# Kernel optimization log

Hardware: AMD Instinct MI355X
Metric: run time of the kernel (lower is better)

## Reference

```python
import jax, jax.numpy as jnp
import numpy as np

# Sizes
N, E = 100000, 3200000
F_NODE, F_EDGE, LD, HID, L = 4, 4, 6, 16, 8
ALPHA = 1.0
EPS = 1e-6


def setup_inputs() -> dict:
    key = jax.random.key(0)
    ks = jax.random.split(key, 8)
    x = jax.random.normal(ks[0], (N, F_NODE), jnp.float32)
    fixed_mask = jax.random.uniform(ks[1], (N,)) < 0.1
    x = x.at[:, -1].set(jnp.where(fixed_mask, jnp.abs(x[:, -1]) + 1.0, 0.0))
    # positive edge attributes (pipe resistance etc.)
    edge_attr = jax.random.uniform(ks[2], (E, F_EDGE), jnp.float32) * 0.9 + 0.1
    edge_index = jax.random.randint(ks[3], (2, E), 0, N, dtype=jnp.int64)
    d_in = 2 * LD + 2 * F_NODE + F_EDGE  # 24: [x_src, x_dst, attr_src, attr_dst, edge_attr]
    s = 0.1
    W1 = jax.random.normal(ks[4], (L, d_in, HID), jnp.float32) * s
    b1 = jnp.zeros((L, HID), jnp.float32)
    W2 = jax.random.normal(ks[5], (L, HID, LD), jnp.float32) * s
    b2 = jnp.zeros((L, LD), jnp.float32)
    Wf = jax.random.normal(ks[6], (LD, 1), jnp.float32) * s
    bf = jnp.zeros((1,), jnp.float32)
    return {"x": x, "edge_attr": edge_attr, "edge_index": edge_index,
            "W1": W1, "b1": b1, "W2": W2, "b2": b2, "Wf": Wf, "bf": bf}


def reference(x, edge_attr, edge_index, W1, b1, W2, b2, Wf, bf):
    src, dst = edge_index[0], edge_index[1]
    # in-degree for mean aggregation
    deg = jax.ops.segment_sum(jnp.ones((E,), jnp.float32), dst, num_segments=N)
    deg = jnp.maximum(deg, 1.0)
    X = jnp.zeros((N, LD), jnp.float32)
    na_src, na_dst = x[src], x[dst]  # static node-attr gathers reused each layer
    for l in range(L):  # num_convs GNNSConv layers
        m_in = jnp.concatenate([X[src], X[dst], na_src, na_dst, edge_attr], axis=-1)  # [E,24]
        h = jax.nn.relu(m_in @ W1[l] + b1[l])         # per-edge MLP hidden [E,16]
        m = h @ W2[l] + b2[l]                          # per-edge message [E,6]
        agg = jax.ops.segment_sum(m, dst, num_segments=N) / deg[:, None]  # mean aggr
        X = (1.0 - ALPHA) * X + ALPHA * agg            # latent update (alpha_update_x)
        X = jax.nn.relu(X)
    P = jax.nn.relu(X @ Wf + bf)                       # [N,1]
    fixed = x[:, -1]
    P_ = jnp.where(fixed != 0, fixed, P.reshape(-1))   # keep known pressures
    # BalanceConv: gas-network flow from squared-pressure drop, k = edge resistance
    dp2 = P_[src] ** 2 - P_[dst] ** 2
    k = edge_attr[:, 0]
    flows = jnp.sign(dp2) * jnp.sqrt(jnp.abs(dp2) / k + EPS)  # [E]
    inj = x[:, 0]  # nodal injection/demand
    balance = (jax.ops.segment_sum(flows, dst, num_segments=N)
               - jax.ops.segment_sum(flows, src, num_segments=N) + inj)
    imbalance = jnp.sqrt(jnp.sum(balance ** 2))
    return P, flows, jnp.stack([imbalance])
```

## Files before the change

### kernel.cpp

```cpp
#include <hip/hip_runtime.h>
#include <math.h>

#define N_NODES 100000
#define N_EDGES 3200000
#define F_NODE 4
#define F_EDGE 4
#define LD 6
#define HID 16
#define NLAYER 8
#define EPSF 1e-6f

#define NPB 64
#define NBK 1563
#define G1 2000
#define CH (N_EDGES / G1)
#define SBK 32
#define CAP 3072

__device__ __forceinline__ unsigned f2bf(float a, float b) {
    unsigned ua = __float_as_uint(a);
    ua = (ua + 0x7fffu + ((ua >> 16) & 1u)) >> 16;
    unsigned ub = __float_as_uint(b);
    ub = (ub + 0x7fffu + ((ub >> 16) & 1u)) & 0xffff0000u;
    return ua | ub;
}
__device__ __forceinline__ float bflo(unsigned u) { return __uint_as_float(u << 16); }
__device__ __forceinline__ float bfhi(unsigned u) { return __uint_as_float(u & 0xffff0000u); }

__global__ __launch_bounds__(256) void hist_kernel(const int* __restrict__ ei,
                                                   int* __restrict__ ghd,
                                                   int* __restrict__ ghs) {
    __shared__ int hd[NBK];
    __shared__ int hs[NBK];
    int t = threadIdx.x;
    for (int i = t; i < NBK; i += 256) { hd[i] = 0; hs[i] = 0; }
    __syncthreads();
    int beg = blockIdx.x * CH, end = beg + CH;
    for (int e = beg + t; e < end; e += 256) {
        atomicAdd(&hs[ei[e] >> 6], 1);
        atomicAdd(&hd[ei[N_EDGES + e] >> 6], 1);
    }
    __syncthreads();
    int* gd = ghd + (size_t)blockIdx.x * NBK;
    int* gs = ghs + (size_t)blockIdx.x * NBK;
    for (int i = t; i < NBK; i += 256) { gd[i] = hd[i]; gs[i] = hs[i]; }
}

__global__ __launch_bounds__(64) void scanb_kernel(int* __restrict__ ghd, int* __restrict__ ghs,
                                                   int* __restrict__ totd, int* __restrict__ tots) {
    int b = blockIdx.x, t = threadIdx.x;
#pragma unroll
    for (int a = 0; a < 2; a++) {
        int* g = a ? ghs : ghd;
        int vals[SBK];
        int sum = 0;
#pragma unroll
        for (int k = 0; k < SBK; k++) {
            int idx = t * SBK + k;
            vals[k] = (idx < G1) ? g[(size_t)idx * NBK + b] : 0;
            sum += vals[k];
        }
        int pre = sum;
        for (int off = 1; off < 64; off <<= 1) { int v = __shfl_up(pre, off, 64); if (t >= off) pre += v; }
        int excl = pre - sum;
        int tot = __shfl(pre, 63, 64);
#pragma unroll
        for (int k = 0; k < SBK; k++) {
            int idx = t * SBK + k;
            if (idx < G1) g[(size_t)idx * NBK + b] = excl;
            excl += vals[k];
        }
        if (t == 0) (a ? tots : totd)[b] = tot;
    }
}

__global__ __launch_bounds__(256) void totscan_kernel(const int* __restrict__ totd,
                                                      const int* __restrict__ tots,
                                                      int* __restrict__ based,
                                                      int* __restrict__ bases) {
    __shared__ int part[256];
    int t = threadIdx.x;
#pragma unroll
    for (int a = 0; a < 2; a++) {
        const int* tot = a ? tots : totd;
        int* base = a ? bases : based;
        int loc[7];
        int sum = 0;
#pragma unroll
        for (int k = 0; k < 7; k++) { int i = t * 7 + k; loc[k] = (i < NBK) ? tot[i] : 0; sum += loc[k]; }
        part[t] = sum;
        __syncthreads();
        for (int off = 1; off < 256; off <<= 1) {
            int v = (t >= off) ? part[t - off] : 0;
            __syncthreads();
            part[t] += v;
            __syncthreads();
        }
        int excl = part[t] - sum;
#pragma unroll
        for (int k = 0; k < 7; k++) { int i = t * 7 + k; if (i < NBK) base[i] = excl; excl += loc[k]; }
        __syncthreads();
    }
}

__global__ __launch_bounds__(256) void scatter_kernel(const int* __restrict__ ei,
                                                      const float* __restrict__ ea,
                                                      const int* __restrict__ ghd,
                                                      const int* __restrict__ ghs,
                                                      const int* __restrict__ based,
                                                      const int* __restrict__ bases,
                                                      uint4* __restrict__ rec,
                                                      unsigned* __restrict__ sbuf) {
    __shared__ int curd[NBK];
    __shared__ int curs[NBK];
    int t = threadIdx.x, blk = blockIdx.x;
    const int* gd = ghd + (size_t)blk * NBK;
    const int* gs = ghs + (size_t)blk * NBK;
    for (int i = t; i < NBK; i += 256) { curd[i] = based[i] + gd[i]; curs[i] = bases[i] + gs[i]; }
    __syncthreads();
    int beg = blk * CH, end = beg + CH;
    for (int e = beg + t; e < end; e += 256) {
        int s = ei[e], d = ei[N_EDGES + e];
        float4 ev = reinterpret_cast<const float4*>(ea)[e];
        int p = atomicAdd(&curd[d >> 6], 1);
        rec[p] = make_uint4((unsigned)s | ((unsigned)(d & 63) << 17),
                            f2bf(ev.x, ev.y), f2bf(ev.z, ev.w), (unsigned)e);
        int q = atomicAdd(&curs[s >> 6], 1);
        sbuf[q] = (unsigned)e | ((unsigned)(s & 63) << 22);
    }
}

__global__ __launch_bounds__(256) void sort_kernel(uint4* __restrict__ rec,
                                                   const int* __restrict__ based,
                                                   const int* __restrict__ totd,
                                                   float* __restrict__ degInv) {
    __shared__ uint4 stage[CAP];
    __shared__ int hist[NPB];
    __shared__ int cur[NPB];
    int b = blockIdx.x, t = threadIdx.x;
    int beg = based[b], tot = totd[b];
    if (t < NPB) hist[t] = 0;
    __syncthreads();
    bool fits = tot <= CAP;
    for (int i = t; i < tot; i += 256) {
        uint4 r = rec[beg + i];
        if (fits) stage[i] = r;
        atomicAdd(&hist[(r.x >> 17) & 63u], 1);
    }
    __syncthreads();
    if (t < NPB) {
        int gid = (b << 6) + t;
        if (gid < N_NODES) degInv[gid] = 1.0f / fmaxf((float)hist[t], 1.0f);
        int v = hist[t];
        int pre = v;
#pragma unroll
        for (int off = 1; off < 64; off <<= 1) {
            int u = __shfl_up(pre, off, 64);
            if (t >= off) pre += u;
        }
        cur[t] = pre - v;
    }
    __syncthreads();
    if (fits) {
        for (int i = t; i < tot; i += 256) {
            uint4 r = stage[i];
            int p = atomicAdd(&cur[(r.x >> 17) & 63u], 1);
            rec[beg + p] = r;
        }
    }
}

__global__ __launch_bounds__(256) void ab_init(const float* __restrict__ x,
                                               const float* __restrict__ W1,
                                               const float* __restrict__ b1,
                                               unsigned* __restrict__ A,
                                               unsigned* __restrict__ B) {
    __shared__ float sW[8 * HID];
    __shared__ float sb[HID];
    int t = threadIdx.x;
    for (int i = t; i < 8 * HID; i += 256) sW[i] = W1[12 * HID + i];
    if (t < HID) sb[t] = b1[t];
    __syncthreads();
    int i = blockIdx.x * 256 + t;
    if (i >= N_NODES) return;
    float4 xv = reinterpret_cast<const float4*>(x)[i];
    float xf[4] = {xv.x, xv.y, xv.z, xv.w};
    float a[HID], bb[HID];
#pragma unroll
    for (int j = 0; j < HID; j++) { a[j] = sb[j]; bb[j] = 0.0f; }
#pragma unroll
    for (int r = 0; r < 4; r++) {
        float v = xf[r];
#pragma unroll
        for (int j = 0; j < HID; j++) {
            a[j]  = fmaf(v, sW[r * HID + j], a[j]);
            bb[j] = fmaf(v, sW[(4 + r) * HID + j], bb[j]);
        }
    }
    uint4* Ao = reinterpret_cast<uint4*>(A + (size_t)i * 8);
    Ao[0] = make_uint4(f2bf(a[0], a[1]), f2bf(a[2], a[3]), f2bf(a[4], a[5]), f2bf(a[6], a[7]));
    Ao[1] = make_uint4(f2bf(a[8], a[9]), f2bf(a[10], a[11]), f2bf(a[12], a[13]), f2bf(a[14], a[15]));
    uint4* Bo = reinterpret_cast<uint4*>(B + (size_t)i * 8);
    Bo[0] = make_uint4(f2bf(bb[0], bb[1]), f2bf(bb[2], bb[3]), f2bf(bb[4], bb[5]), f2bf(bb[6], bb[7]));
    Bo[1] = make_uint4(f2bf(bb[8], bb[9]), f2bf(bb[10], bb[11]), f2bf(bb[12], bb[13]), f2bf(bb[14], bb[15]));
}

template <int LAST>
__global__ __launch_bounds__(256) void edge_layer(const uint4* __restrict__ rec,
                                                  const unsigned* __restrict__ Ain,
                                                  const unsigned* __restrict__ Bin,
                                                  const float* __restrict__ x,
                                                  const float* __restrict__ degInv,
                                                  const float* __restrict__ W1l,
                                                  const float* __restrict__ W2l,
                                                  const float* __restrict__ b2l,
                                                  const float* __restrict__ W1n,
                                                  const float* __restrict__ b1n,
                                                  const float* __restrict__ Wf,
                                                  const float* __restrict__ bfp,
                                                  const int* __restrict__ based,
                                                  const int* __restrict__ totd,
                                                  unsigned* __restrict__ Aout,
                                                  unsigned* __restrict__ Bout,
                                                  float* __restrict__ Pout,
                                                  float* __restrict__ Pbuf) {
    __shared__ float sWea[4 * HID];
    __shared__ float sW2[HID * LD];
    __shared__ float sb2[LD];
    __shared__ float sW1n[20 * HID];
    __shared__ float sb1n[HID];
    __shared__ float sWf[LD];
    __shared__ float sbf;
    __shared__ float accf[LD * NPB];
    __shared__ unsigned sB[NPB * 8];
    int t = threadIdx.x;
    int b = blockIdx.x;
    for (int i = t; i < 4 * HID; i += 256) sWea[i] = W1l[20 * HID + i];
    for (int i = t; i < HID * LD; i += 256) sW2[i] = W2l[i];
    if (t < LD) sb2[t] = b2l[t];
    if (!LAST) {
        for (int i = t; i < 20 * HID; i += 256) sW1n[i] = W1n[i];
        if (t < HID) sb1n[t] = b1n[t];
    } else {
        if (t < LD) sWf[t] = Wf[t];
        if (t == 0) sbf = bfp[0];
    }
    for (int i = t; i < LD * NPB; i += 256) accf[i] = 0.0f;
    {
        size_t base8 = (size_t)(b << 6) * 8;
        for (int i = t; i < NPB * 8; i += 256) {
            size_t gi = base8 + i;
            sB[i] = (gi < (size_t)N_NODES * 8) ? Bin[gi] : 0u;
        }
    }
    __syncthreads();

    int beg = based[b], tot = totd[b];
    int end = beg + tot;
    int lane = t & 63;

    for (int base = beg; base < end; base += 256) {
        int p = base + t;
        bool valid = p < end;
        int key = -1;
        float out[LD];
#pragma unroll
        for (int o = 0; o < LD; o++) out[o] = 0.0f;

        if (valid) {
            uint4 r = rec[p];
            int s = (int)(r.x & 0x1FFFFu);
            key = (int)((r.x >> 17) & 63u);
            const uint4* Ap = reinterpret_cast<const uint4*>(Ain + (size_t)s * 8);
            uint4 ax = Ap[0], ay = Ap[1];
            const uint4* Bp = reinterpret_cast<const uint4*>(sB) + key * 2;
            uint4 bx = Bp[0], by = Bp[1];
            float h[HID];
            h[0]  = bflo(ax.x) + bflo(bx.x);  h[1]  = bfhi(ax.x) + bfhi(bx.x);
            h[2]  = bflo(ax.y) + bflo(bx.y);  h[3]  = bfhi(ax.y) + bfhi(bx.y);
            h[4]  = bflo(ax.z) + bflo(bx.z);  h[5]  = bfhi(ax.z) + bfhi(bx.z);
            h[6]  = bflo(ax.w) + bflo(bx.w);  h[7]  = bfhi(ax.w) + bfhi(bx.w);
            h[8]  = bflo(ay.x) + bflo(by.x);  h[9]  = bfhi(ay.x) + bfhi(by.x);
            h[10] = bflo(ay.y) + bflo(by.y);  h[11] = bfhi(ay.y) + bfhi(by.y);
            h[12] = bflo(ay.z) + bflo(by.z);  h[13] = bfhi(ay.z) + bfhi(by.z);
            h[14] = bflo(ay.w) + bflo(by.w);  h[15] = bfhi(ay.w) + bfhi(by.w);
            float ef[4] = {bflo(r.y), bfhi(r.y), bflo(r.z), bfhi(r.z)};
#pragma unroll
            for (int rr = 0; rr < 4; rr++) {
                float v = ef[rr];
#pragma unroll
                for (int j = 0; j < HID; j++) h[j] = fmaf(v, sWea[rr * HID + j], h[j]);
            }
#pragma unroll
            for (int j = 0; j < HID; j++) h[j] = fmaxf(h[j], 0.0f);
#pragma unroll
            for (int o = 0; o < LD; o++) out[o] = sb2[o];
#pragma unroll
            for (int j = 0; j < HID; j++) {
                float hj = h[j];
#pragma unroll
                for (int o = 0; o < LD; o++) out[o] = fmaf(hj, sW2[j * LD + o], out[o]);
            }
        }

#pragma unroll
        for (int st = 1; st < 64; st <<= 1) {
            int kup = __shfl_up(key, st, 64);
            bool same = (lane >= st) && (kup == key);
#pragma unroll
            for (int o = 0; o < LD; o++) {
                float v = __shfl_up(out[o], st, 64);
                if (same) out[o] += v;
            }
        }
        int knx = __shfl_down(key, 1, 64);
        bool tail = (lane == 63) || (knx != key);
        if (valid && tail) {
#pragma unroll
            for (int o = 0; o < LD; o++) atomicAdd(&accf[o * NPB + key], out[o]);
        }
    }
    __syncthreads();

    if (t < NPB) {
        int gid = (b << 6) + t;
        if (gid < N_NODES) {
            float inv = degInv[gid];
            float Xv[LD];
#pragma unroll
            for (int o = 0; o < LD; o++) Xv[o] = fmaxf(accf[o * NPB + t] * inv, 0.0f);
            if (LAST) {
                float a2 = sbf;
#pragma unroll
                for (int o = 0; o < LD; o++) a2 = fmaf(Xv[o], sWf[o], a2);
                float P = fmaxf(a2, 0.0f);
                Pout[gid] = P;
                float fx = x[gid * F_NODE + 3];
                Pbuf[gid] = (fx != 0.0f) ? fx : P;
            } else {
                float4 xv = reinterpret_cast<const float4*>(x)[gid];
                float xf[4] = {xv.x, xv.y, xv.z, xv.w};
                float a[HID], bb[HID];
#pragma unroll
                for (int j = 0; j < HID; j++) { a[j] = sb1n[j]; bb[j] = 0.0f; }
#pragma unroll
                for (int rr = 0; rr < LD; rr++) {
                    float v = Xv[rr];
#pragma unroll
                    for (int j = 0; j < HID; j++) {
                        a[j]  = fmaf(v, sW1n[rr * HID + j], a[j]);
                        bb[j] = fmaf(v, sW1n[(LD + rr) * HID + j], bb[j]);
                    }
                }
#pragma unroll
                for (int rr = 0; rr < 4; rr++) {
                    float v = xf[rr];
#pragma unroll
                    for (int j = 0; j < HID; j++) {
                        a[j]  = fmaf(v, sW1n[(12 + rr) * HID + j], a[j]);
                        bb[j] = fmaf(v, sW1n[(16 + rr) * HID + j], bb[j]);
                    }
                }
                uint4* Ao = reinterpret_cast<uint4*>(Aout + (size_t)gid * 8);
                Ao[0] = make_uint4(f2bf(a[0], a[1]), f2bf(a[2], a[3]), f2bf(a[4], a[5]), f2bf(a[6], a[7]));
                Ao[1] = make_uint4(f2bf(a[8], a[9]), f2bf(a[10], a[11]), f2bf(a[12], a[13]), f2bf(a[14], a[15]));
                uint4* Bo = reinterpret_cast<uint4*>(Bout + (size_t)gid * 8);
                Bo[0] = make_uint4(f2bf(bb[0], bb[1]), f2bf(bb[2], bb[3]), f2bf(bb[4], bb[5]), f2bf(bb[6], bb[7]));
                Bo[1] = make_uint4(f2bf(bb[8], bb[9]), f2bf(bb[10], bb[11]), f2bf(bb[12], bb[13]), f2bf(bb[14], bb[15]));
            }
        }
    }
}

__global__ __launch_bounds__(256) void flows_noatomic(const int* __restrict__ ei,
                                                      const float* __restrict__ ea,
                                                      const float* __restrict__ Pbuf,
                                                      float* __restrict__ flows_out) {
    int e = blockIdx.x * 256 + threadIdx.x;
    if (e >= N_EDGES) return;
    int s = ei[e];
    int d = ei[N_EDGES + e];
    float ps = Pbuf[s], pd = Pbuf[d];
    float dp2 = ps * ps - pd * pd;
    float k = ea[(size_t)e * F_EDGE];
    float sg = (dp2 > 0.0f) ? 1.0f : ((dp2 < 0.0f) ? -1.0f : 0.0f);
    flows_out[e] = sg * sqrtf(fabsf(dp2) / k + EPSF);
}

__global__ __launch_bounds__(256) void balance_in(const uint4* __restrict__ rec,
                                                  const float* __restrict__ flows,
                                                  const float* __restrict__ x,
                                                  const int* __restrict__ based,
                                                  const int* __restrict__ totd,
                                                  float* __restrict__ bal) {
    __shared__ float acc[NPB];
    int t = threadIdx.x;
    if (t < NPB) acc[t] = 0.0f;
    __syncthreads();
    int b = blockIdx.x;
    int beg = based[b], end = beg + totd[b];
    int lane = t & 63;
    for (int base = beg; base < end; base += 256) {
        int p = base + t;
        bool valid = p < end;
        int key = -1;
        float f = 0.0f;
        if (valid) {
            uint4 r = rec[p];
            key = (int)((r.x >> 17) & 63u);
            f = flows[r.w];
        }
#pragma unroll
        for (int st = 1; st < 64; st <<= 1) {
            int kup = __shfl_up(key, st, 64);
            float v = __shfl_up(f, st, 64);
            if ((lane >= st) && (kup == key)) f += v;
        }
        int knx = __shfl_down(key, 1, 64);
        bool tail = (lane == 63) || (knx != key);
        if (valid && tail) atomicAdd(&acc[key], f);
    }
    __syncthreads();
    if (t < NPB) {
        int gid = (b << 6) + t;
        if (gid < N_NODES) bal[gid] = acc[t] + x[gid * F_NODE + 0];
    }
}

__global__ __launch_bounds__(256) void balance_out(const unsigned* __restrict__ sbuf,
                                                   const float* __restrict__ flows,
                                                   const int* __restrict__ bases,
                                                   const int* __restrict__ tots,
                                                   const float* __restrict__ bal,
                                                   float* __restrict__ imb2) {
    __shared__ float acc[NPB];
    int t = threadIdx.x;
    if (t < NPB) acc[t] = 0.0f;
    __syncthreads();
    int b = blockIdx.x;
    int beg = bases[b], end = beg + tots[b];
    for (int q = beg + t; q < end; q += 256) {
        unsigned u = sbuf[q];
        atomicAdd(&acc[(u >> 22) & 63u], flows[u & 0x3FFFFFu]);
    }
    __syncthreads();
    if (t < NPB) {
        float v = 0.0f;
        int gid = (b << 6) + t;
        if (gid < N_NODES) {
            float bv = bal[gid] - acc[t];
            v = bv * bv;
        }
#pragma unroll
        for (int off = 32; off > 0; off >>= 1) v += __shfl_down(v, off, 64);
        if (t == 0) atomicAdd(imb2, v);
    }
}

__global__ void fin_kernel(const float* __restrict__ imb2, float* __restrict__ out) {
    out[0] = sqrtf(imb2[0]);
}

extern "C" void kernel_launch(void* const* d_in, const int* in_sizes, int n_in,
                              void* d_out, int out_size, void* d_ws, size_t ws_size,
                              hipStream_t stream) {
    const float* x   = (const float*)d_in[0];
    const float* ea  = (const float*)d_in[1];
    const int*   ei  = (const int*)d_in[2];
    const float* W1  = (const float*)d_in[3];
    const float* b1  = (const float*)d_in[4];
    const float* W2  = (const float*)d_in[5];
    const float* b2  = (const float*)d_in[6];
    const float* Wf  = (const float*)d_in[7];
    const float* bf_ = (const float*)d_in[8];
    float* out = (float*)d_out;

    const size_t N = N_NODES, E = N_EDGES;

    size_t o = 0;
    auto alloc = [&](size_t n) { size_t r = o; o += (n + 3) & ~(size_t)3; return r; };
    size_t o_rec    = alloc(4 * E);
    size_t o_sbuf   = alloc(E);
    size_t o_ghd    = alloc((size_t)G1 * NBK);
    size_t o_ghs    = alloc((size_t)G1 * NBK);
    size_t o_totd   = alloc(NBK);
    size_t o_tots   = alloc(NBK);
    size_t o_based  = alloc(NBK);
    size_t o_bases  = alloc(NBK);
    size_t o_degInv = alloc(N);
    size_t o_A0     = alloc(8 * N);
    size_t o_B0     = alloc(8 * N);
    size_t o_A1     = alloc(8 * N);
    size_t o_B1     = alloc(8 * N);
    size_t o_Pbuf   = alloc(N);
    size_t o_bal    = alloc(N);
    size_t o_imb2   = alloc(16);
    (void)o;

    int* wsi = (int*)d_ws;
    uint4*    rec    = (uint4*)(wsi + o_rec);
    unsigned* sbuf   = (unsigned*)(wsi + o_sbuf);
    int*      ghd    = wsi + o_ghd;
    int*      ghs    = wsi + o_ghs;
    int*      totd   = wsi + o_totd;
    int*      tots   = wsi + o_tots;
    int*      based  = wsi + o_based;
    int*      bases  = wsi + o_bases;
    float*    degInv = (float*)(wsi + o_degInv);
    unsigned* A0     = (unsigned*)(wsi + o_A0);
    unsigned* B0     = (unsigned*)(wsi + o_B0);
    unsigned* A1     = (unsigned*)(wsi + o_A1);
    unsigned* B1     = (unsigned*)(wsi + o_B1);
    float*    Pbuf   = (float*)(wsi + o_Pbuf);
    float*    bal    = (float*)(wsi + o_bal);
    float*    imb2   = (float*)(wsi + o_imb2);

    const int NB = (N_NODES + 255) / 256;
    const int EB = (N_EDGES + 255) / 256;

    hipMemsetAsync(imb2, 0, sizeof(float), stream);

    hist_kernel<<<G1, 256, 0, stream>>>(ei, ghd, ghs);
    scanb_kernel<<<NBK, 64, 0, stream>>>(ghd, ghs, totd, tots);
    totscan_kernel<<<1, 256, 0, stream>>>(totd, tots, based, bases);
    scatter_kernel<<<G1, 256, 0, stream>>>(ei, ea, ghd, ghs, based, bases, rec, sbuf);
    sort_kernel<<<NBK, 256, 0, stream>>>(rec, based, totd, degInv);

    ab_init<<<NB, 256, 0, stream>>>(x, W1, b1, A0, B0);

    for (int l = 0; l < NLAYER; l++) {
        const unsigned* Ain = (l & 1) ? A1 : A0;
        const unsigned* Bin = (l & 1) ? B1 : B0;
        unsigned* Aout = (l & 1) ? A0 : A1;
        unsigned* Bout = (l & 1) ? B0 : B1;
        const float* W1l = W1 + (size_t)l * 24 * HID;
        const float* W2l = W2 + (size_t)l * HID * LD;
        const float* b2l = b2 + (size_t)l * LD;
        if (l < NLAYER - 1) {
            edge_layer<0><<<NBK, 256, 0, stream>>>(rec, Ain, Bin, x, degInv, W1l, W2l, b2l,
                                                   W1 + (size_t)(l + 1) * 24 * HID,
                                                   b1 + (size_t)(l + 1) * HID,
                                                   Wf, bf_, based, totd,
                                                   Aout, Bout, out, Pbuf);
        } else {
            edge_layer<1><<<NBK, 256, 0, stream>>>(rec, Ain, Bin, x, degInv, W1l, W2l, b2l,
                                                   W1, b1, Wf, bf_, based, totd,
                                                   Aout, Bout, out, Pbuf);
        }
    }

    flows_noatomic<<<EB, 256, 0, stream>>>(ei, ea, Pbuf, out + N);
    balance_in<<<NBK, 256, 0, stream>>>(rec, out + N, x, based, totd, bal);
    balance_out<<<NBK, 256, 0, stream>>>(sbuf, out + N, bases, tots, bal, imb2);
    fin_kernel<<<1, 1, 0, stream>>>(imb2, out + (size_t)N + E);
}
```

Baseline: 923.8 us.

## Restructure edge sort into coarse 512-node bins with full per-node ordering

The counting sort now uses 196 coarse 512-node bins with transposed histograms, and a second in-bin pass fully orders edges by destination node (and source edges by source node) while packing edge attributes. The edge layer stages record tiles in shared memory and gives each thread a contiguous run of sorted edges. It accumulates per node in registers, flushing to shared memory only when the node changes, which replaces the wavefront shuffle segmented scan. The aim is fewer histogram and scan costs, fewer atomics and less shuffle work per layer, at the cost of an extra sort pass, more shared memory per block, and possible load imbalance across threads.

Result: slower. 944.2 us (+2.2%).

```diff
diff --git a/kernel.cpp b/kernel.cpp
--- a/kernel.cpp
+++ b/kernel.cpp
@@ -12,10 +12,10 @@
 
 #define NPB 64
 #define NBK 1563
+#define NBIN 196
 #define G1 2000
 #define CH (N_EDGES / G1)
-#define SBK 32
-#define CAP 3072
+#define TILE 2048
 
 __device__ __forceinline__ unsigned f2bf(float a, float b) {
     unsigned ua = __float_as_uint(a);
@@ -30,64 +30,38 @@
 __global__ __launch_bounds__(256) void hist_kernel(const int* __restrict__ ei,
                                                    int* __restrict__ ghd,
                                                    int* __restrict__ ghs) {
-    __shared__ int hd[NBK];
-    __shared__ int hs[NBK];
-    int t = threadIdx.x;
-    for (int i = t; i < NBK; i += 256) { hd[i] = 0; hs[i] = 0; }
-    __syncthreads();
-    int beg = blockIdx.x * CH, end = beg + CH;
+    __shared__ int hd[NBIN];
+    __shared__ int hs[NBIN];
+    int t = threadIdx.x, blk = blockIdx.x;
+    for (int i = t; i < NBIN; i += 256) { hd[i] = 0; hs[i] = 0; }
+    __syncthreads();
+    int beg = blk * CH, end = beg + CH;
     for (int e = beg + t; e < end; e += 256) {
-        atomicAdd(&hs[ei[e] >> 6], 1);
-        atomicAdd(&hd[ei[N_EDGES + e] >> 6], 1);
-    }
-    __syncthreads();
-    int* gd = ghd + (size_t)blockIdx.x * NBK;
-    int* gs = ghs + (size_t)blockIdx.x * NBK;
-    for (int i = t; i < NBK; i += 256) { gd[i] = hd[i]; gs[i] = hs[i]; }
-}
-
-__global__ __launch_bounds__(64) void scanb_kernel(int* __restrict__ ghd, int* __restrict__ ghs,
-                                                   int* __restrict__ totd, int* __restrict__ tots) {
+        atomicAdd(&hs[ei[e] >> 9], 1);
+        atomicAdd(&hd[ei[N_EDGES + e] >> 9], 1);
+    }
+    __syncthreads();
+    for (int i = t; i < NBIN; i += 256) {
+        ghd[(size_t)i * G1 + blk] = hd[i];
+        ghs[(size_t)i * G1 + blk] = hs[i];
+    }
+}
+
+__global__ __launch_bounds__(256) void scanb_kernel(int* __restrict__ ghd, int* __restrict__ ghs,
+                                                    int* __restrict__ totd, int* __restrict__ tots) {
+    __shared__ int part[256];
     int b = blockIdx.x, t = threadIdx.x;
 #pragma unroll
     for (int a = 0; a < 2; a++) {
         int* g = a ? ghs : ghd;
-        int vals[SBK];
+        int vals[8];
         int sum = 0;
 #pragma unroll
-        for (int k = 0; k < SBK; k++) {
-            int idx = t * SBK + k;
-            vals[k] = (idx < G1) ? g[(size_t)idx * NBK + b] : 0;
+        for (int k = 0; k < 8; k++) {
+            int idx = t * 8 + k;
+            vals[k] = (idx < G1) ? g[(size_t)b * G1 + idx] : 0;
             sum += vals[k];
         }
-        int pre = sum;
-        for (int off = 1; off < 64; off <<= 1) { int v = __shfl_up(pre, off, 64); if (t >= off) pre += v; }
-        int excl = pre - sum;
-        int tot = __shfl(pre, 63, 64);
-#pragma unroll
-        for (int k = 0; k < SBK; k++) {
-            int idx = t * SBK + k;
-            if (idx < G1) g[(size_t)idx * NBK + b] = excl;
-            excl += vals[k];
-        }
-        if (t == 0) (a ? tots : totd)[b] = tot;
-    }
-}
-
-__global__ __launch_bounds__(256) void totscan_kernel(const int* __restrict__ totd,
-                                                      const int* __restrict__ tots,
-                                                      int* __restrict__ based,
-                                                      int* __restrict__ bases) {
-    __shared__ int part[256];
-    int t = threadIdx.x;
-#pragma unroll
-    for (int a = 0; a < 2; a++) {
-        const int* tot = a ? tots : totd;
-        int* base = a ? bases : based;
-        int loc[7];
-        int sum = 0;
-#pragma unroll
-        for (int k = 0; k < 7; k++) { int i = t * 7 + k; loc[k] = (i < NBK) ? tot[i] : 0; sum += loc[k]; }
         part[t] = sum;
         __syncthreads();
         for (int off = 1; off < 256; off <<= 1) {
@@ -98,75 +72,160 @@
         }
         int excl = part[t] - sum;
 #pragma unroll
-        for (int k = 0; k < 7; k++) { int i = t * 7 + k; if (i < NBK) base[i] = excl; excl += loc[k]; }
-        __syncthreads();
-    }
-}
-
-__global__ __launch_bounds__(256) void scatter_kernel(const int* __restrict__ ei,
-                                                      const float* __restrict__ ea,
-                                                      const int* __restrict__ ghd,
-                                                      const int* __restrict__ ghs,
-                                                      const int* __restrict__ based,
-                                                      const int* __restrict__ bases,
-                                                      uint4* __restrict__ rec,
-                                                      unsigned* __restrict__ sbuf) {
-    __shared__ int curd[NBK];
-    __shared__ int curs[NBK];
+        for (int k = 0; k < 8; k++) {
+            int idx = t * 8 + k;
+            if (idx < G1) g[(size_t)b * G1 + idx] = excl;
+            excl += vals[k];
+        }
+        if (t == 0) (a ? tots : totd)[b] = part[255];
+        __syncthreads();
+    }
+}
+
+__global__ __launch_bounds__(256) void totscan_kernel(const int* __restrict__ totd,
+                                                      const int* __restrict__ tots,
+                                                      int* __restrict__ binbased,
+                                                      int* __restrict__ binbases) {
+    __shared__ int part[256];
+    int t = threadIdx.x;
+#pragma unroll
+    for (int a = 0; a < 2; a++) {
+        const int* tot = a ? tots : totd;
+        int* base = a ? binbases : binbased;
+        int v = (t < NBIN) ? tot[t] : 0;
+        part[t] = v;
+        __syncthreads();
+        for (int off = 1; off < 256; off <<= 1) {
+            int u = (t >= off) ? part[t - off] : 0;
+            __syncthreads();
+            part[t] += u;
+            __syncthreads();
+        }
+        if (t < NBIN) base[t] = part[t] - v;
+        if (t == 0) base[NBIN] = N_EDGES;
+        __syncthreads();
+    }
+}
+
+__global__ __launch_bounds__(256) void scatterA_kernel(const int* __restrict__ ei,
+                                                       const int* __restrict__ ghd,
+                                                       const int* __restrict__ ghs,
+                                                       const int* __restrict__ binbased,
+                                                       const int* __restrict__ binbases,
+                                                       uint2* __restrict__ recA,
+                                                       unsigned* __restrict__ sbufA) {
+    __shared__ int curd[NBIN];
+    __shared__ int curs[NBIN];
     int t = threadIdx.x, blk = blockIdx.x;
-    const int* gd = ghd + (size_t)blk * NBK;
-    const int* gs = ghs + (size_t)blk * NBK;
-    for (int i = t; i < NBK; i += 256) { curd[i] = based[i] + gd[i]; curs[i] = bases[i] + gs[i]; }
+    for (int i = t; i < NBIN; i += 256) {
+        curd[i] = binbased[i] + ghd[(size_t)i * G1 + blk];
+        curs[i] = binbases[i] + ghs[(size_t)i * G1 + blk];
+    }
     __syncthreads();
     int beg = blk * CH, end = beg + CH;
     for (int e = beg + t; e < end; e += 256) {
         int s = ei[e], d = ei[N_EDGES + e];
+        int p = atomicAdd(&curd[d >> 9], 1);
+        recA[p] = make_uint2((unsigned)s | ((unsigned)(d & 511) << 17), (unsigned)e);
+        int q = atomicAdd(&curs[s >> 9], 1);
+        sbufA[q] = (unsigned)e | ((unsigned)(s & 511) << 22);
+    }
+}
+
+__global__ __launch_bounds__(256) void sortrec_kernel(const uint2* __restrict__ recA,
+                                                      const float* __restrict__ ea,
+                                                      const int* __restrict__ binbased,
+                                                      uint4* __restrict__ recB,
+                                                      float* __restrict__ degInv,
+                                                      int* __restrict__ based_bk) {
+    __shared__ int hist[512];
+    __shared__ int cur[512];
+    __shared__ int part[256];
+    int b = blockIdx.x, t = threadIdx.x;
+    hist[t] = 0;
+    hist[t + 256] = 0;
+    __syncthreads();
+    int beg = binbased[b], end = binbased[b + 1];
+    for (int i = beg + t; i < end; i += 256)
+        atomicAdd(&hist[(recA[i].x >> 17) & 511u], 1);
+    __syncthreads();
+    int s0 = hist[2 * t], s1 = hist[2 * t + 1];
+    int tsum = s0 + s1;
+    part[t] = tsum;
+    __syncthreads();
+    for (int off = 1; off < 256; off <<= 1) {
+        int v = (t >= off) ? part[t - off] : 0;
+        __syncthreads();
+        part[t] += v;
+        __syncthreads();
+    }
+    int excl = part[t] - tsum;
+    cur[2 * t] = beg + excl;
+    cur[2 * t + 1] = beg + excl + s0;
+    __syncthreads();
+    int node0 = b << 9;
+    for (int j = t; j < 512; j += 256) {
+        int node = node0 + j;
+        if (node < N_NODES) degInv[node] = 1.0f / fmaxf((float)hist[j], 1.0f);
+    }
+    if (t < 8) {
+        int node = node0 + t * 64;
+        if (node < N_NODES) based_bk[(b << 3) + t] = cur[t * 64];
+    }
+    if (b == NBIN - 1 && t == 0) based_bk[NBK] = N_EDGES;
+    __syncthreads();
+    for (int i = beg + t; i < end; i += 256) {
+        uint2 r = recA[i];
+        int nib = (int)((r.x >> 17) & 511u);
+        unsigned s = r.x & 0x1FFFFu;
+        unsigned e = r.y;
+        int p = atomicAdd(&cur[nib], 1);
         float4 ev = reinterpret_cast<const float4*>(ea)[e];
-        int p = atomicAdd(&curd[d >> 6], 1);
-        rec[p] = make_uint4((unsigned)s | ((unsigned)(d & 63) << 17),
-                            f2bf(ev.x, ev.y), f2bf(ev.z, ev.w), (unsigned)e);
-        int q = atomicAdd(&curs[s >> 6], 1);
-        sbuf[q] = (unsigned)e | ((unsigned)(s & 63) << 22);
-    }
-}
-
-__global__ __launch_bounds__(256) void sort_kernel(uint4* __restrict__ rec,
-                                                   const int* __restrict__ based,
-                                                   const int* __restrict__ totd,
-                                                   float* __restrict__ degInv) {
-    __shared__ uint4 stage[CAP];
-    __shared__ int hist[NPB];
-    __shared__ int cur[NPB];
+        recB[p] = make_uint4(s | ((unsigned)(nib & 63) << 17),
+                             f2bf(ev.x, ev.y), f2bf(ev.z, ev.w), e);
+    }
+}
+
+__global__ __launch_bounds__(256) void sortsrc_kernel(const unsigned* __restrict__ sbufA,
+                                                      const int* __restrict__ binbases,
+                                                      unsigned* __restrict__ sbufB,
+                                                      int* __restrict__ bases_bk) {
+    __shared__ int hist[512];
+    __shared__ int cur[512];
+    __shared__ int part[256];
     int b = blockIdx.x, t = threadIdx.x;
-    int beg = based[b], tot = totd[b];
-    if (t < NPB) hist[t] = 0;
-    __syncthreads();
-    bool fits = tot <= CAP;
-    for (int i = t; i < tot; i += 256) {
-        uint4 r = rec[beg + i];
-        if (fits) stage[i] = r;
-        atomicAdd(&hist[(r.x >> 17) & 63u], 1);
-    }
-    __syncthreads();
-    if (t < NPB) {
-        int gid = (b << 6) + t;
-        if (gid < N_NODES) degInv[gid] = 1.0f / fmaxf((float)hist[t], 1.0f);
-        int v = hist[t];
-        int pre = v;
-#pragma unroll
-        for (int off = 1; off < 64; off <<= 1) {
-            int u = __shfl_up(pre, off, 64);
-            if (t >= off) pre += u;
-        }
-        cur[t] = pre - v;
-    }
-    __syncthreads();
-    if (fits) {
-        for (int i = t; i < tot; i += 256) {
-            uint4 r = stage[i];
-            int p = atomicAdd(&cur[(r.x >> 17) & 63u], 1);
-            rec[beg + p] = r;
-        }
+    hist[t] = 0;
+    hist[t + 256] = 0;
+    __syncthreads();
+    int beg = binbases[b], end = binbases[b + 1];
+    for (int i = beg + t; i < end; i += 256)
+        atomicAdd(&hist[(sbufA[i] >> 22) & 511u], 1);
+    __syncthreads();
+    int s0 = hist[2 * t], s1 = hist[2 * t + 1];
+    int tsum = s0 + s1;
+    part[t] = tsum;
+    __syncthreads();
+    for (int off = 1; off < 256; off <<= 1) {
+        int v = (t >= off) ? part[t - off] : 0;
+        __syncthreads();
+        part[t] += v;
+        __syncthreads();
+    }
+    int excl = part[t] - tsum;
+    cur[2 * t] = beg + excl;
+    cur[2 * t + 1] = beg + excl + s0;
+    __syncthreads();
+    if (t < 8) {
+        int node = (b << 9) + t * 64;
+        if (node < N_NODES) bases_bk[(b << 3) + t] = cur[t * 64];
+    }
+    if (b == NBIN - 1 && t == 0) bases_bk[NBK] = N_EDGES;
+    __syncthreads();
+    for (int i = beg + t; i < end; i += 256) {
+        unsigned w = sbufA[i];
+        int nib = (int)((w >> 22) & 511u);
+        int p = atomicAdd(&cur[nib], 1);
+        sbufB[p] = (w & 0x3FFFFFu) | ((unsigned)(nib & 63) << 22);
     }
 }
 
@@ -206,7 +265,7 @@
 }
 
 template <int LAST>
-__global__ __launch_bounds__(256) void edge_layer(const uint4* __restrict__ rec,
+__global__ __launch_bounds__(256) void edge_layer(const uint4* __restrict__ recB,
                                                   const unsigned* __restrict__ Ain,
                                                   const unsigned* __restrict__ Bin,
                                                   const float* __restrict__ x,
@@ -218,8 +277,7 @@
                                                   const float* __restrict__ b1n,
                                                   const float* __restrict__ Wf,
                                                   const float* __restrict__ bfp,
-                                                  const int* __restrict__ based,
-                                                  const int* __restrict__ totd,
+                                                  const int* __restrict__ based_bk,
                                                   unsigned* __restrict__ Aout,
                                                   unsigned* __restrict__ Bout,
                                                   float* __restrict__ Pout,
@@ -233,6 +291,7 @@
     __shared__ float sbf;
     __shared__ float accf[LD * NPB];
     __shared__ unsigned sB[NPB * 8];
+    __shared__ uint4 tile[TILE];
     int t = threadIdx.x;
     int b = blockIdx.x;
     for (int i = t; i < 4 * HID; i += 256) sWea[i] = W1l[20 * HID + i];
@@ -255,26 +314,41 @@
     }
     __syncthreads();
 
-    int beg = based[b], tot = totd[b];
-    int end = beg + tot;
-    int lane = t & 63;
-
-    for (int base = beg; base < end; base += 256) {
-        int p = base + t;
-        bool valid = p < end;
-        int key = -1;
-        float out[LD];
-#pragma unroll
-        for (int o = 0; o < LD; o++) out[o] = 0.0f;
-
-        if (valid) {
-            uint4 r = rec[p];
+    int beg = based_bk[b], end = based_bk[b + 1];
+
+    for (int base = beg; base < end; base += TILE) {
+        int m = end - base;
+        if (m > TILE) m = TILE;
+        for (int i = t; i < m; i += 256) tile[i] = recB[base + i];
+        __syncthreads();
+        int K2 = (m + 255) >> 8;
+        int q0 = t * K2;
+        int q1 = q0 + K2;
+        if (q1 > m) q1 = m;
+        float acc[LD];
+        int cur = -1;
+        uint4 bx, by;
+#pragma unroll
+        for (int o = 0; o < LD; o++) acc[o] = 0.0f;
+#pragma unroll 2
+        for (int q = q0; q < q1; ++q) {
+            uint4 r = tile[q];
+            int dl = (int)((r.x >> 17) & 63u);
+            if (dl != cur) {
+                if (cur >= 0) {
+#pragma unroll
+                    for (int o = 0; o < LD; o++) atomicAdd(&accf[o * NPB + cur], acc[o]);
+                }
+                cur = dl;
+#pragma unroll
+                for (int o = 0; o < LD; o++) acc[o] = 0.0f;
+                const uint4* Bp = reinterpret_cast<const uint4*>(sB) + dl * 2;
+                bx = Bp[0];
+                by = Bp[1];
+            }
             int s = (int)(r.x & 0x1FFFFu);
-            key = (int)((r.x >> 17) & 63u);
             const uint4* Ap = reinterpret_cast<const uint4*>(Ain + (size_t)s * 8);
             uint4 ax = Ap[0], ay = Ap[1];
-            const uint4* Bp = reinterpret_cast<const uint4*>(sB) + key * 2;
-            uint4 bx = Bp[0], by = Bp[1];
             float h[HID];
             h[0]  = bflo(ax.x) + bflo(bx.x);  h[1]  = bfhi(ax.x) + bfhi(bx.x);
             h[2]  = bflo(ax.y) + bflo(bx.y);  h[3]  = bfhi(ax.y) + bfhi(bx.y);
@@ -293,34 +367,24 @@
             }
 #pragma unroll
             for (int j = 0; j < HID; j++) h[j] = fmaxf(h[j], 0.0f);
-#pragma unroll
-            for (int o = 0; o < LD; o++) out[o] = sb2[o];
+            float mo[LD];
+#pragma unroll
+            for (int o = 0; o < LD; o++) mo[o] = sb2[o];
 #pragma unroll
             for (int j = 0; j < HID; j++) {
                 float hj = h[j];
 #pragma unroll
-                for (int o = 0; o < LD; o++) out[o] = fmaf(hj, sW2[j * LD + o], out[o]);
+                for (int o = 0; o < LD; o++) mo[o] = fmaf(hj, sW2[j * LD + o], mo[o]);
             }
-        }
-
-#pragma unroll
-        for (int st = 1; st < 64; st <<= 1) {
-            int kup = __shfl_up(key, st, 64);
-            bool same = (lane >= st) && (kup == key);
-#pragma unroll
-            for (int o = 0; o < LD; o++) {
-                float v = __shfl_up(out[o], st, 64);
-                if (same) out[o] += v;
-            }
-        }
-        int knx = __shfl_down(key, 1, 64);
-        bool tail = (lane == 63) || (knx != key);
-        if (valid && tail) {
-#pragma unroll
-            for (int o = 0; o < LD; o++) atomicAdd(&accf[o * NPB + key], out[o]);
-        }
-    }
-    __syncthreads();
+#pragma unroll
+            for (int o = 0; o < LD; o++) acc[o] += mo[o];
+        }
+        if (cur >= 0) {
+#pragma unroll
+            for (int o = 0; o < LD; o++) atomicAdd(&accf[o * NPB + cur], acc[o]);
+        }
+        __syncthreads();
+    }
 
     if (t < NPB) {
         int gid = (b << 6) + t;
@@ -387,18 +451,17 @@
     flows_out[e] = sg * sqrtf(fabsf(dp2) / k + EPSF);
 }
 
-__global__ __launch_bounds__(256) void balance_in(const uint4* __restrict__ rec,
+__global__ __launch_bounds__(256) void balance_in(const uint4* __restrict__ recB,
                                                   const float* __restrict__ flows,
                                                   const float* __restrict__ x,
-                                                  const int* __restrict__ based,
-                                                  const int* __restrict__ totd,
+                                                  const int* __restrict__ based_bk,
                                                   float* __restrict__ bal) {
     __shared__ float acc[NPB];
     int t = threadIdx.x;
     if (t < NPB) acc[t] = 0.0f;
     __syncthreads();
     int b = blockIdx.x;
-    int beg = based[b], end = beg + totd[b];
+    int beg = based_bk[b], end = based_bk[b + 1];
     int lane = t & 63;
     for (int base = beg; base < end; base += 256) {
         int p = base + t;
@@ -406,7 +469,7 @@
         int key = -1;
         float f = 0.0f;
         if (valid) {
-            uint4 r = rec[p];
+            uint4 r = recB[p];
             key = (int)((r.x >> 17) & 63u);
             f = flows[r.w];
         }
@@ -427,10 +490,9 @@
     }
 }
 
-__global__ __launch_bounds__(256) void balance_out(const unsigned* __restrict__ sbuf,
+__global__ __launch_bounds__(256) void balance_out(const unsigned* __restrict__ sbufB,
                                                    const float* __restrict__ flows,
-                                                   const int* __restrict__ bases,
-                                                   const int* __restrict__ tots,
+                                                   const int* __restrict__ bases_bk,
                                                    const float* __restrict__ bal,
                                                    float* __restrict__ imb2) {
     __shared__ float acc[NPB];
@@ -438,10 +500,27 @@
     if (t < NPB) acc[t] = 0.0f;
     __syncthreads();
     int b = blockIdx.x;
-    int beg = bases[b], end = beg + tots[b];
-    for (int q = beg + t; q < end; q += 256) {
-        unsigned u = sbuf[q];
-        atomicAdd(&acc[(u >> 22) & 63u], flows[u & 0x3FFFFFu]);
+    int beg = bases_bk[b], end = bases_bk[b + 1];
+    int lane = t & 63;
+    for (int base = beg; base < end; base += 256) {
+        int q = base + t;
+        bool valid = q < end;
+        int key = -1;
+        float f = 0.0f;
+        if (valid) {
+            unsigned u = sbufB[q];
+            key = (int)((u >> 22) & 63u);
+            f = flows[u & 0x3FFFFFu];
+        }
+#pragma unroll
+        for (int st = 1; st < 64; st <<= 1) {
+            int kup = __shfl_up(key, st, 64);
+            float v = __shfl_up(f, st, 64);
+            if ((lane >= st) && (kup == key)) f += v;
+        }
+        int knx = __shfl_down(key, 1, 64);
+        bool tail = (lane == 63) || (knx != key);
+        if (valid && tail) atomicAdd(&acc[key], f);
     }
     __syncthreads();
     if (t < NPB) {
@@ -479,41 +558,48 @@
 
     size_t o = 0;
     auto alloc = [&](size_t n) { size_t r = o; o += (n + 3) & ~(size_t)3; return r; };
-    size_t o_rec    = alloc(4 * E);
-    size_t o_sbuf   = alloc(E);
-    size_t o_ghd    = alloc((size_t)G1 * NBK);
-    size_t o_ghs    = alloc((size_t)G1 * NBK);
-    size_t o_totd   = alloc(NBK);
-    size_t o_tots   = alloc(NBK);
-    size_t o_based  = alloc(NBK);
-    size_t o_bases  = alloc(NBK);
-    size_t o_degInv = alloc(N);
-    size_t o_A0     = alloc(8 * N);
-    size_t o_B0     = alloc(8 * N);
-    size_t o_A1     = alloc(8 * N);
-    size_t o_B1     = alloc(8 * N);
-    size_t o_Pbuf   = alloc(N);
-    size_t o_bal    = alloc(N);
-    size_t o_imb2   = alloc(16);
+    size_t o_recB     = alloc(4 * E);
+    size_t o_recA     = alloc(2 * E);
+    size_t o_sbufA    = alloc(E);
+    size_t o_ghd      = alloc((size_t)NBIN * G1);
+    size_t o_ghs      = alloc((size_t)NBIN * G1);
+    size_t o_totd     = alloc(NBIN);
+    size_t o_tots     = alloc(NBIN);
+    size_t o_binbased = alloc(NBIN + 1);
+    size_t o_binbases = alloc(NBIN + 1);
+    size_t o_basedbk  = alloc(NBK + 1);
+    size_t o_basesbk  = alloc(NBK + 1);
+    size_t o_degInv   = alloc(N);
+    size_t o_A0       = alloc(8 * N);
+    size_t o_B0       = alloc(8 * N);
+    size_t o_A1       = alloc(8 * N);
+    size_t o_B1       = alloc(8 * N);
+    size_t o_Pbuf     = alloc(N);
+    size_t o_bal      = alloc(N);
+    size_t o_imb2     = alloc(16);
     (void)o;
 
     int* wsi = (int*)d_ws;
-    uint4*    rec    = (uint4*)(wsi + o_rec);
-    unsigned* sbuf   = (unsigned*)(wsi + o_sbuf);
-    int*      ghd    = wsi + o_ghd;
-    int*      ghs    = wsi + o_ghs;
-    int*      totd   = wsi + o_totd;
-    int*      tots   = wsi + o_tots;
-    int*      based  = wsi + o_based;
-    int*      bases  = wsi + o_bases;
-    float*    degInv = (float*)(wsi + o_degInv);
-    unsigned* A0     = (unsigned*)(wsi + o_A0);
-    unsigned* B0     = (unsigned*)(wsi + o_B0);
-    unsigned* A1     = (unsigned*)(wsi + o_A1);
-    unsigned* B1     = (unsigned*)(wsi + o_B1);
-    float*    Pbuf   = (float*)(wsi + o_Pbuf);
-    float*    bal    = (float*)(wsi + o_bal);
-    float*    imb2   = (float*)(wsi + o_imb2);
+    uint4*    recB     = (uint4*)(wsi + o_recB);
+    uint2*    recA     = (uint2*)(wsi + o_recA);
+    unsigned* sbufA    = (unsigned*)(wsi + o_sbufA);
+    unsigned* sbufB    = (unsigned*)(wsi + o_recA);
+    int*      ghd      = wsi + o_ghd;
+    int*      ghs      = wsi + o_ghs;
+    int*      totd     = wsi + o_totd;
+    int*      tots     = wsi + o_tots;
+    int*      binbased = wsi + o_binbased;
+    int*      binbases = wsi + o_binbases;
+    int*      based_bk = wsi + o_basedbk;
+    int*      bases_bk = wsi + o_basesbk;
+    float*    degInv   = (float*)(wsi + o_degInv);
+    unsigned* A0       = (unsigned*)(wsi + o_A0);
+    unsigned* B0       = (unsigned*)(wsi + o_B0);
+    unsigned* A1       = (unsigned*)(wsi + o_A1);
+    unsigned* B1       = (unsigned*)(wsi + o_B1);
+    float*    Pbuf     = (float*)(wsi + o_Pbuf);
+    float*    bal      = (float*)(wsi + o_bal);
+    float*    imb2     = (float*)(wsi + o_imb2);
 
     const int NB = (N_NODES + 255) / 256;
     const int EB = (N_EDGES + 255) / 256;
@@ -521,10 +607,11 @@
     hipMemsetAsync(imb2, 0, sizeof(float), stream);
 
     hist_kernel<<<G1, 256, 0, stream>>>(ei, ghd, ghs);
-    scanb_kernel<<<NBK, 64, 0, stream>>>(ghd, ghs, totd, tots);
-    totscan_kernel<<<1, 256, 0, stream>>>(totd, tots, based, bases);
-    scatter_kernel<<<G1, 256, 0, stream>>>(ei, ea, ghd, ghs, based, bases, rec, sbuf);
-    sort_kernel<<<NBK, 256, 0, stream>>>(rec, based, totd, degInv);
+    scanb_kernel<<<NBIN, 256, 0, stream>>>(ghd, ghs, totd, tots);
+    totscan_kernel<<<1, 256, 0, stream>>>(totd, tots, binbased, binbases);
+    scatterA_kernel<<<G1, 256, 0, stream>>>(ei, ghd, ghs, binbased, binbases, recA, sbufA);
+    sortrec_kernel<<<NBIN, 256, 0, stream>>>(recA, ea, binbased, recB, degInv, based_bk);
+    sortsrc_kernel<<<NBIN, 256, 0, stream>>>(sbufA, binbases, sbufB, bases_bk);
 
     ab_init<<<NB, 256, 0, stream>>>(x, W1, b1, A0, B0);
 
@@ -537,20 +624,20 @@
         const float* W2l = W2 + (size_t)l * HID * LD;
         const float* b2l = b2 + (size_t)l * LD;
         if (l < NLAYER - 1) {
-            edge_layer<0><<<NBK, 256, 0, stream>>>(rec, Ain, Bin, x, degInv, W1l, W2l, b2l,
+            edge_layer<0><<<NBK, 256, 0, stream>>>(recB, Ain, Bin, x, degInv, W1l, W2l, b2l,
                                                    W1 + (size_t)(l + 1) * 24 * HID,
                                                    b1 + (size_t)(l + 1) * HID,
-                                                   Wf, bf_, based, totd,
+                                                   Wf, bf_, based_bk,
                                                    Aout, Bout, out, Pbuf);
         } else {
-            edge_layer<1><<<NBK, 256, 0, stream>>>(rec, Ain, Bin, x, degInv, W1l, W2l, b2l,
-                                                   W1, b1, Wf, bf_, based, totd,
+            edge_layer<1><<<NBK, 256, 0, stream>>>(recB, Ain, Bin, x, degInv, W1l, W2l, b2l,
+                                                   W1, b1, Wf, bf_, based_bk,
                                                    Aout, Bout, out, Pbuf);
         }
     }
 
     flows_noatomic<<<EB, 256, 0, stream>>>(ei, ea, Pbuf, out + N);
-    balance_in<<<NBK, 256, 0, stream>>>(rec, out + N, x, based, totd, bal);
-    balance_out<<<NBK, 256, 0, stream>>>(sbuf, out + N, bases, tots, bal, imb2);
+    balance_in<<<NBK, 256, 0, stream>>>(recB, out + N, x, based_bk, bal);
+    balance_out<<<NBK, 256, 0, stream>>>(sbufB, out + N, bases_bk, bal, imb2);
     fin_kernel<<<1, 1, 0, stream>>>(imb2, out + (size_t)N + E);
 }
```
